# Performance work log

Hardware: AMD Instinct MI355X
Metric: run time of the kernel (lower is better)

Reference implementation:

```python
import jax, jax.numpy as jnp
import numpy as np
import math

N = 256  # channels == model dim M
B, H, W = 8, 48, 48
EPS = 1e-5


def _kaiming(key, shape, a=math.sqrt(5)):
    # kaiming_normal_ with fan_in = shape[1] (2D weight), leaky_relu gain
    fan_in = shape[1]
    gain = math.sqrt(2.0 / (1.0 + a * a))
    std = gain / math.sqrt(fan_in)
    return std * jax.random.normal(key, shape, dtype=jnp.float32)


def setup_inputs() -> dict:
    key = jax.random.key(0)
    ks = jax.random.split(key, 6)
    x_l = jax.random.normal(ks[0], (B, N, H, W), dtype=jnp.float32)
    x_r = jax.random.normal(ks[1], (B, N, H, W), dtype=jnp.float32)
    Wq = _kaiming(ks[2], (N, N))
    Wk = _kaiming(ks[3], (N, N))
    Wv = _kaiming(ks[4], (N, N))
    Wo = _kaiming(ks[5], (N, N))
    g1 = jnp.ones((N,), jnp.float32); b1 = jnp.zeros((N,), jnp.float32)
    g2 = jnp.ones((N,), jnp.float32); b2 = jnp.zeros((N,), jnp.float32)
    return {"x_l": x_l, "x_r": x_r, "Wq": Wq, "Wk": Wk, "Wv": Wv, "Wo": Wo,
            "g1": g1, "b1": b1, "g2": g2, "b2": b2}


def _layernorm(x, g, b):
    mu = jnp.mean(x, axis=-1, keepdims=True)
    var = jnp.mean(jnp.square(x - mu), axis=-1, keepdims=True)
    return (x - mu) * jax.lax.rsqrt(var + EPS) * g + b


def reference(x_l, x_r, Wq, Wk, Wv, Wo, g1, b1, g2, b2):
    Bsz, C, Hh, Ww = x_l.shape
    S = Hh * Ww
    # [B, C, H, W] -> [B, S, C]
    xl = x_l.reshape(Bsz, C, S).transpose(0, 2, 1)
    xr = x_r.reshape(Bsz, C, S).transpose(0, 2, 1)
    xln_l = _layernorm(xl, g1, b1)
    xln_r = _layernorm(xr, g2, b2)
    Ql = xln_l @ Wq; Qr = xln_r @ Wq
    Kl = xln_l @ Wk; Kr = xln_r @ Wk
    Vl = xln_l @ Wv; Vr = xln_r @ Wv
    scale = 1.0 / math.sqrt(C)
    Al = jnp.einsum('bsc,btc->bst', Ql, Kr) * scale  # [B,S,S]
    Ar = jnp.einsum('bsc,btc->bst', Qr, Kl) * scale
    # NOTE: original uses nn.Softmax() with dim=None; for a 3-D tensor torch's
    # legacy _get_softmax_dim resolves to dim=0 (over batch). Faithfully replicated.
    Pl = jax.nn.softmax(Al, axis=0)
    Pr = jax.nn.softmax(Ar, axis=0)
    out_l = xl + (Pl @ Vl) @ Wo
    out_r = xr + (Pr @ Vr) @ Wo
    out_l = out_l.transpose(0, 2, 1).reshape(Bsz, C, Hh, Ww)
    out_r = out_r.transpose(0, 2, 1).reshape(Bsz, C, Hh, Ww)
    return out_l, out_r
```

## Files before the change

kernel.cpp:

```cpp
#include <hip/hip_runtime.h>
#include <stdint.h>

#define SDIM 2304
#define CDIM 256
#define NB   8
#define MTOT (NB * SDIM)

typedef __attribute__((ext_vector_type(8))) short short8;
typedef __attribute__((ext_vector_type(4))) float f32x4;

__device__ __forceinline__ float b2f(unsigned short h) {
  union { unsigned int u; float f; } v; v.u = ((unsigned int)h) << 16; return v.f;
}
__device__ __forceinline__ unsigned short f2b(float f) {
  union { unsigned int u; float f; } v; v.f = f;
  unsigned int u = v.u;
  u += 0x7fffu + ((u >> 16) & 1u);
  return (unsigned short)(u >> 16);
}
static inline unsigned short f2b_host(float f) {
  union { unsigned int u; float f; } v; v.f = f;
  unsigned int u = v.u;
  u += 0x7fffu + ((u >> 16) & 1u);
  return (unsigned short)(u >> 16);
}

__device__ __forceinline__ void gload_lds16(const unsigned short* g, unsigned short* l) {
  __builtin_amdgcn_global_load_lds(
      (const __attribute__((address_space(1))) unsigned int*)g,
      (__attribute__((address_space(3))) unsigned int*)l,
      16, 0, 0);
}

__global__ __launch_bounds__(64)
void detect_dtype(const unsigned short* __restrict__ x, int* __restrict__ flag)
{
  int lane = threadIdx.x;
  int bad = 0;
  for (int i = lane; i < 1024; i += 64) {
    float v = b2f(x[i]);
    if (!(fabsf(v) < 1e20f)) bad = 1;
  }
  unsigned long long m = __ballot(bad);
  if (lane == 0) flag[0] = (m != 0ULL) ? 1 : 0;
}

constexpr int EP_PLAIN = 0, EP_QKV = 1, EP_OUT = 2, EP_ACC = 3;

template <int EP, int SW>
__global__ __launch_bounds__(256, 2)
void gemm_nt(const unsigned short* __restrict__ pA, int lda, long sAz,
             const unsigned short* __restrict__ pB, int ldb, long sBz, int zx,
             unsigned short* __restrict__ pC, int ldc, long sCz,
             unsigned short* __restrict__ pQ, unsigned short* __restrict__ pK,
             unsigned short* __restrict__ pV,
             const unsigned short* __restrict__ pX0, const unsigned short* __restrict__ pX1,
             float* __restrict__ pFacc, unsigned short* __restrict__ pBf, int accmode,
             const int* __restrict__ dflag, int Kdim)
{
  __shared__ __align__(16) unsigned short As[3][128 * 32];
  __shared__ __align__(16) unsigned short Bs[3][128 * 32];

  const int tid = threadIdx.x;
  int bx, by, bz;
  if constexpr (SW == 1) {
    const int h = blockIdx.x;
    const int q = h >> 4, r = h & 15;
    const int p = q * 8 + (r & 7);
    by = r >> 3;
    bx = p % 18;
    bz = p / 18;
  } else {
    bx = blockIdx.x; by = blockIdx.y; bz = blockIdx.z;
  }
  const int z = bz;
  const long m0 = (long)bx * 128;
  const long n0 = (long)by * 128;
  const unsigned short* A  = pA + (long)z * sAz;
  const unsigned short* Bm = pB + (long)(z ^ zx) * sBz;

  const int lane = tid & 63;
  const int wave = tid >> 6;
  const int wm = (wave & 1) << 6;
  const int wn = (wave >> 1) << 6;
  const int lr = lane & 15;
  const int quad = lane >> 4;

  f32x4 acc[4][4];
#pragma unroll
  for (int i = 0; i < 4; ++i)
#pragma unroll
    for (int j = 0; j < 4; ++j) acc[i][j] = (f32x4)0.0f;

  const int e0 = tid, e1 = tid + 256;
  const int r0 = e0 >> 2, c0 = (e0 & 3) << 3;
  const int r1 = e1 >> 2, c1 = (e1 & 3) << 3;
  const unsigned short* pa0 = A  + (m0 + r0) * lda + c0;
  const unsigned short* pa1 = A  + (m0 + r1) * lda + c1;
  const unsigned short* pb0 = Bm + (n0 + r0) * ldb + c0;
  const unsigned short* pb1 = Bm + (n0 + r1) * ldb + c1;

  const int nt = Kdim >> 5;

  gload_lds16(pa0,      &As[0][e0 * 8]);
  gload_lds16(pa1,      &As[0][e1 * 8]);
  gload_lds16(pb0,      &Bs[0][e0 * 8]);
  gload_lds16(pb1,      &Bs[0][e1 * 8]);
  gload_lds16(pa0 + 32, &As[1][e0 * 8]);
  gload_lds16(pa1 + 32, &As[1][e1 * 8]);
  gload_lds16(pb0 + 32, &Bs[1][e0 * 8]);
  gload_lds16(pb1 + 32, &Bs[1][e1 * 8]);

  int bc = 0;
  for (int t = 0; t < nt; ++t) {
    if (t < nt - 1) asm volatile("s_waitcnt vmcnt(4)" ::: "memory");
    else            asm volatile("s_waitcnt vmcnt(0)" ::: "memory");
    __builtin_amdgcn_s_barrier();
    asm volatile("" ::: "memory");

    if (t + 2 < nt) {
      const int k2 = (t + 2) << 5;
      const int b2 = bc ? bc - 1 : 2;
      gload_lds16(pa0 + k2, &As[b2][e0 * 8]);
      gload_lds16(pa1 + k2, &As[b2][e1 * 8]);
      gload_lds16(pb0 + k2, &Bs[b2][e0 * 8]);
      gload_lds16(pb1 + k2, &Bs[b2][e1 * 8]);
    }

    short8 af[4], bfr[4];
#pragma unroll
    for (int i = 0; i < 4; ++i) {
      af[i]  = *(const short8*)&As[bc][(wm + i * 16 + lr) * 32 + quad * 8];
      bfr[i] = *(const short8*)&Bs[bc][(wn + i * 16 + lr) * 32 + quad * 8];
    }
#pragma unroll
    for (int i = 0; i < 4; ++i)
#pragma unroll
      for (int j = 0; j < 4; ++j)
        acc[i][j] = __builtin_amdgcn_mfma_f32_16x16x32_bf16(af[i], bfr[j], acc[i][j], 0, 0, 0);

    bc = (bc == 2) ? 0 : bc + 1;
  }

  if constexpr (EP == EP_PLAIN) {
    unsigned short* Cp = pC + (long)z * sCz;
#pragma unroll
    for (int i = 0; i < 4; ++i) {
      const long mb = m0 + wm + i * 16 + quad * 4;
#pragma unroll
      for (int j = 0; j < 4; ++j) {
        const long n = n0 + wn + j * 16 + lr;
#pragma unroll
        for (int r = 0; r < 4; ++r)
          Cp[(mb + r) * ldc + n] = f2b(acc[i][j][r]);
      }
    }
  } else if constexpr (EP == EP_QKV) {
    const int g  = (int)(n0 >> 8);
    const int nb = (int)(n0 & 255);
    if (g < 2) {
      unsigned short* Cp = (g == 0 ? pQ : pK) + (long)z * sCz;
#pragma unroll
      for (int i = 0; i < 4; ++i) {
        const long mb = m0 + wm + i * 16 + quad * 4;
#pragma unroll
        for (int j = 0; j < 4; ++j) {
          const int n = nb + wn + j * 16 + lr;
#pragma unroll
          for (int r = 0; r < 4; ++r)
            Cp[(mb + r) * CDIM + n] = f2b(acc[i][j][r]);
        }
      }
    } else {
      const int b = (int)(m0 / SDIM);
      const int sblk = (int)(m0 % SDIM);
      unsigned short* Vz = pV + ((long)z * NB + b) * (long)CDIM * SDIM;
#pragma unroll
      for (int i = 0; i < 4; ++i) {
        const int s = sblk + wm + i * 16 + quad * 4;
#pragma unroll
        for (int j = 0; j < 4; ++j) {
          const int c = nb + wn + j * 16 + lr;
          ushort4 pk;
          pk.x = f2b(acc[i][j][0]); pk.y = f2b(acc[i][j][1]);
          pk.z = f2b(acc[i][j][2]); pk.w = f2b(acc[i][j][3]);
          *(ushort4*)&Vz[(long)c * SDIM + s] = pk;
        }
      }
    }
  } else if constexpr (EP == EP_ACC) {
    float* Fz = pFacc + (long)z * SDIM * CDIM;
    unsigned short* Bz = pBf + (long)z * SDIM * CDIM;
#pragma unroll
    for (int i = 0; i < 4; ++i) {
      const long mb = m0 + wm + i * 16 + quad * 4;
#pragma unroll
      for (int j = 0; j < 4; ++j) {
        const long n = n0 + wn + j * 16 + lr;
#pragma unroll
        for (int r = 0; r < 4; ++r) {
          const long idx = (mb + r) * CDIM + n;
          float v = acc[i][j][r];
          if (accmode != 0) v += Fz[idx];
          if (accmode == 2) Bz[idx] = f2b(v);
          else              Fz[idx] = v;
        }
      }
    }
  } else {
    const int io32 = dflag[0];
    const int b = (int)(m0 / SDIM);
    const int sblk = (int)(m0 % SDIM);
    const unsigned short* Xraw = (z == 0 ? pX0 : pX1);
    if (io32) {
      const float* Xf = (const float*)Xraw + (long)b * CDIM * SDIM;
      float* Of = (float*)pC + (long)z * sCz + (long)b * CDIM * SDIM;
#pragma unroll
      for (int i = 0; i < 4; ++i) {
        const int s = sblk + wm + i * 16 + quad * 4;
#pragma unroll
        for (int j = 0; j < 4; ++j) {
          const int c = (int)n0 + wn + j * 16 + lr;
          const long off = (long)c * SDIM + s;
          float4 rx = *(const float4*)&Xf[off];
          float4 pk;
          pk.x = acc[i][j][0] + rx.x;
          pk.y = acc[i][j][1] + rx.y;
          pk.z = acc[i][j][2] + rx.z;
          pk.w = acc[i][j][3] + rx.w;
          *(float4*)&Of[off] = pk;
        }
      }
    } else {
      const unsigned short* X = Xraw + (long)b * CDIM * SDIM;
      unsigned short* O = pC + (long)z * sCz + (long)b * CDIM * SDIM;
#pragma unroll
      for (int i = 0; i < 4; ++i) {
        const int s = sblk + wm + i * 16 + quad * 4;
#pragma unroll
        for (int j = 0; j < 4; ++j) {
          const int c = (int)n0 + wn + j * 16 + lr;
          const long off = (long)c * SDIM + s;
          ushort4 rx = *(const ushort4*)&X[off];
          ushort4 pk;
          pk.x = f2b(acc[i][j][0] + b2f(rx.x));
          pk.y = f2b(acc[i][j][1] + b2f(rx.y));
          pk.z = f2b(acc[i][j][2] + b2f(rx.z));
          pk.w = f2b(acc[i][j][3] + b2f(rx.w));
          *(ushort4*)&O[off] = pk;
        }
      }
    }
  }
}

__global__ __launch_bounds__(256)
void wtrans(const unsigned short* __restrict__ Wq, const unsigned short* __restrict__ Wk,
            const unsigned short* __restrict__ Wv, const unsigned short* __restrict__ Wo,
            unsigned short* __restrict__ WT, const int* __restrict__ dflag)
{
  const int io32 = dflag[0];
  int idx = blockIdx.x * 256 + threadIdx.x;
  int w = idx >> 16, r = idx & 65535, n = r >> 8, k = r & 255;
  const unsigned short* W = (w == 0) ? Wq : (w == 1) ? Wk : (w == 2) ? Wv : Wo;
  float v = io32 ? ((const float*)W)[k * 256 + n] : b2f(W[k * 256 + n]);
  if (w == 0) v *= 0.0625f;
  WT[w * 65536 + n * 256 + k] = f2b(v);
}

__global__ __launch_bounds__(256)
void ln_kernel(const unsigned short* __restrict__ xl, const unsigned short* __restrict__ xr,
               const unsigned short* __restrict__ g1, const unsigned short* __restrict__ b1,
               const unsigned short* __restrict__ g2, const unsigned short* __restrict__ b2,
               unsigned short* __restrict__ XLN, const int* __restrict__ dflag)
{
  const int io32 = dflag[0];
  const int strm = blockIdx.z;
  const int b = blockIdx.y;
  const int s0 = blockIdx.x * 64;
  const unsigned short* xraw = (strm ? xr : xl);
  const float*          xf = (const float*)xraw + (long)b * CDIM * SDIM;
  const unsigned short* xh = xraw + (long)b * CDIM * SDIM;
  const unsigned short* gg = strm ? g2 : g1;
  const unsigned short* bb = strm ? b2 : b1;
  const int tid = threadIdx.x;
  const int sl = tid & 63;
  const int team = tid >> 6;

  __shared__ float red[2][4][64];
  __shared__ float muS[64], rsS[64];
  __shared__ __align__(16) unsigned short tile[64 * 258];

  float sum = 0.f, sq = 0.f;
  for (int c = team * 64; c < team * 64 + 64; ++c) {
    const long off = (long)c * SDIM + s0 + sl;
    float v = io32 ? xf[off] : b2f(xh[off]);
    sum += v; sq += v * v;
  }
  red[0][team][sl] = sum; red[1][team][sl] = sq;
  __syncthreads();
  if (tid < 64) {
    float s_ = red[0][0][tid] + red[0][1][tid] + red[0][2][tid] + red[0][3][tid];
    float q_ = red[1][0][tid] + red[1][1][tid] + red[1][2][tid] + red[1][3][tid];
    float mu = s_ * (1.0f / CDIM);
    float var = q_ * (1.0f / CDIM) - mu * mu;
    muS[tid] = mu;
    rsS[tid] = rsqrtf(var + 1e-5f);
  }
  __syncthreads();
  const float mu = muS[sl], rs = rsS[sl];
  for (int c = team * 64; c < team * 64 + 64; ++c) {
    const long off = (long)c * SDIM + s0 + sl;
    float v = io32 ? xf[off] : b2f(xh[off]);
    float gv = io32 ? ((const float*)gg)[c] : b2f(gg[c]);
    float bv = io32 ? ((const float*)bb)[c] : b2f(bb[c]);
    tile[sl * 258 + c] = f2b((v - mu) * rs * gv + bv);
  }
  __syncthreads();
  unsigned short* outp = XLN + ((long)strm * MTOT + (long)b * SDIM + s0) * CDIM;
  const ushort2* t2 = (const ushort2*)tile;
  ushort2* o2 = (ushort2*)outp;
#pragma unroll
  for (int i = 0; i < 32; ++i) {
    int idx = i * 256 + tid;
    int r = idx >> 7, c2 = idx & 127;
    o2[idx] = t2[r * 129 + c2];
  }
}

__global__ __launch_bounds__(256)
void softmax_bdim(unsigned short* __restrict__ Ab, long total)
{
  const int strm = blockIdx.y;
  const long i8 = (((long)blockIdx.x << 8) + threadIdx.x) << 3;
  unsigned short* base = Ab + (long)strm * NB * total + i8;
  float v[NB][8];
#pragma unroll
  for (int b = 0; b < NB; ++b) {
    const ushort4* p = (const ushort4*)(base + (long)b * total);
    ushort4 a0 = p[0], a1 = p[1];
    v[b][0] = b2f(a0.x); v[b][1] = b2f(a0.y); v[b][2] = b2f(a0.z); v[b][3] = b2f(a0.w);
    v[b][4] = b2f(a1.x); v[b][5] = b2f(a1.y); v[b][6] = b2f(a1.z); v[b][7] = b2f(a1.w);
  }
#pragma unroll
  for (int j = 0; j < 8; ++j) {
    float mx = v[0][j];
#pragma unroll
    for (int b = 1; b < NB; ++b) mx = fmaxf(mx, v[b][j]);
    float s = 0.f;
#pragma unroll
    for (int b = 0; b < NB; ++b) { float e = __expf(v[b][j] - mx); v[b][j] = e; s += e; }
    float inv = 1.0f / s;
#pragma unroll
    for (int b = 0; b < NB; ++b) v[b][j] *= inv;
  }
#pragma unroll
  for (int b = 0; b < NB; ++b) {
    ushort4 a0, a1;
    a0.x = f2b(v[b][0]); a0.y = f2b(v[b][1]); a0.z = f2b(v[b][2]); a0.w = f2b(v[b][3]);
    a1.x = f2b(v[b][4]); a1.y = f2b(v[b][5]); a1.z = f2b(v[b][6]); a1.w = f2b(v[b][7]);
    ushort4* p = (ushort4*)(base + (long)b * total);
    p[0] = a0; p[1] = a1;
  }
}

__global__ __launch_bounds__(256)
void fill_val(unsigned short* __restrict__ out, unsigned short v, int n)
{
  int i = blockIdx.x * 256 + threadIdx.x;
  if (i < n) out[i] = v;
}

extern "C" void kernel_launch(void* const* d_in, const int* in_sizes, int n_in,
                              void* d_out, int out_size, void* d_ws, size_t ws_size,
                              hipStream_t stream)
{
  const unsigned short* xl = (const unsigned short*)d_in[0];
  const unsigned short* xr = (const unsigned short*)d_in[1];
  const unsigned short* Wq = (const unsigned short*)d_in[2];
  const unsigned short* Wk = (const unsigned short*)d_in[3];
  const unsigned short* Wv = (const unsigned short*)d_in[4];
  const unsigned short* Wo = (const unsigned short*)d_in[5];
  const unsigned short* g1 = (const unsigned short*)d_in[6];
  const unsigned short* b1 = (const unsigned short*)d_in[7];
  const unsigned short* g2 = (const unsigned short*)d_in[8];
  const unsigned short* b2 = (const unsigned short*)d_in[9];
  unsigned short* out = (unsigned short*)d_out;

  const size_t need_chunk = 113770496UL + 64;
  const size_t need_full  = 227016704UL + 64;
  if (ws_size < need_chunk) {
    float wsmb = (float)(ws_size >> 20);
    unsigned short v = f2b_host(wsmb * 100.0f);
    fill_val<<<dim3((out_size + 255) / 256), 256, 0, stream>>>(out, v, out_size);
    return;
  }

  int* dFlag = (int*)((char*)d_ws + ((ws_size - 16) & ~15UL));
  detect_dtype<<<dim3(1), 64, 0, stream>>>(xl, dFlag);

  if (ws_size >= need_full) {
    unsigned short* WT  = (unsigned short*)d_ws;
    unsigned short* Qb  = WT + 262144L;
    unsigned short* Kb  = Qb + 9437184L;
    unsigned short* Vt  = Kb + 9437184L;
    unsigned short* Ab  = Vt + 9437184L;
    unsigned short* XLN = Ab;
    unsigned short* PVbf = Qb;

    wtrans<<<dim3(1024), 256, 0, stream>>>(Wq, Wk, Wv, Wo, WT, dFlag);
    ln_kernel<<<dim3(36, 8, 2), 256, 0, stream>>>(xl, xr, g1, b1, g2, b2, XLN, dFlag);

    gemm_nt<EP_QKV, 0><<<dim3(144, 6, 2), 256, 0, stream>>>(
        XLN, CDIM, (long)MTOT * CDIM,
        WT, CDIM, 0L, 0,
        nullptr, 0, (long)MTOT * CDIM,
        Qb, Kb, Vt, nullptr, nullptr,
        nullptr, nullptr, 0, dFlag, CDIM);

    gemm_nt<EP_PLAIN, 0><<<dim3(18, 18, 16), 256, 0, stream>>>(
        Qb, CDIM, (long)SDIM * CDIM,
        Kb, CDIM, (long)SDIM * CDIM, 8,
        Ab, SDIM, (long)SDIM * SDIM,
        nullptr, nullptr, nullptr, nullptr, nullptr,
        nullptr, nullptr, 0, dFlag, CDIM);

    softmax_bdim<<<dim3(2592, 2), 256, 0, stream>>>(Ab, (long)SDIM * SDIM);

    gemm_nt<EP_PLAIN, 1><<<dim3(576), 256, 0, stream>>>(
        Ab, SDIM, (long)SDIM * SDIM,
        Vt, SDIM, (long)CDIM * SDIM, 0,
        PVbf, CDIM, (long)SDIM * CDIM,
        nullptr, nullptr, nullptr, nullptr, nullptr,
        nullptr, nullptr, 0, dFlag, SDIM);

    gemm_nt<EP_OUT, 0><<<dim3(144, 2, 2), 256, 0, stream>>>(
        PVbf, CDIM, (long)MTOT * CDIM,
        WT + 768L * 256, CDIM, 0L, 0,
        out, 0, (long)NB * CDIM * SDIM,
        nullptr, nullptr, nullptr, xl, xr,
        nullptr, nullptr, 0, dFlag, CDIM);
    return;
  }

  unsigned short* WT  = (unsigned short*)d_ws;
  unsigned short* XLN = WT  + 1024L * 256;
  unsigned short* Abc = XLN;
  unsigned short* Qb  = XLN + 9437184L;
  unsigned short* Kb  = Qb  + 9437184L;
  unsigned short* Vt  = Kb  + 9437184L;
  float*          PVacc = (float*)(Vt + 9437184L);
  unsigned short* PVbf  = Qb;

  wtrans<<<dim3(1024), 256, 0, stream>>>(Wq, Wk, Wv, Wo, WT, dFlag);
  ln_kernel<<<dim3(36, 8, 2), 256, 0, stream>>>(xl, xr, g1, b1, g2, b2, XLN, dFlag);

  gemm_nt<EP_QKV, 0><<<dim3(144, 6, 2), 256, 0, stream>>>(
      XLN, CDIM, (long)MTOT * CDIM,
      WT, CDIM, 0L, 0,
      nullptr, 0, (long)MTOT * CDIM,
      Qb, Kb, Vt, nullptr, nullptr,
      nullptr, nullptr, 0, dFlag, CDIM);

  for (int tc = 0; tc < 9; ++tc) {
    gemm_nt<EP_PLAIN, 0><<<dim3(18, 2, 16), 256, 0, stream>>>(
        Qb, CDIM, (long)SDIM * CDIM,
        Kb + (long)tc * 256 * CDIM, CDIM, (long)SDIM * CDIM, 8,
        Abc, 256, (long)SDIM * 256,
        nullptr, nullptr, nullptr, nullptr, nullptr,
        nullptr, nullptr, 0, dFlag, CDIM);

    softmax_bdim<<<dim3(288, 2), 256, 0, stream>>>(Abc, (long)SDIM * 256);

    const int mode = (tc == 0) ? 0 : (tc == 8) ? 2 : 1;
    gemm_nt<EP_ACC, 0><<<dim3(18, 2, 16), 256, 0, stream>>>(
        Abc, 256, (long)SDIM * 256,
        Vt + (long)tc * 256, SDIM, (long)CDIM * SDIM, 0,
        nullptr, 0, 0L,
        nullptr, nullptr, nullptr, nullptr, nullptr,
        PVacc, PVbf, mode, dFlag, 256);
  }

  gemm_nt<EP_OUT, 0><<<dim3(144, 2, 2), 256, 0, stream>>>(
      PVbf, CDIM, (long)MTOT * CDIM,
      WT + 768L * 256, CDIM, 0L, 0,
      out, 0, (long)NB * CDIM * SDIM,
      nullptr, nullptr, nullptr, xl, xr,
      nullptr, nullptr, 0, dFlag, CDIM);
}
```

Measured before the change: 388.7 us.

## Fuse QK^T GEMM with batch-dim softmax into a single kernel

Replaces the separate QK^T GEMM and batch-axis softmax kernels with one kernel. Each block computes a 128x64 score tile for all 8 batches, keeps the bf16 results packed in registers, applies the softmax over the batch dimension in registers, and writes the probabilities once. This removes one full write-and-reread round trip of the large score tensor. In exchange it uses many registers (the packed score array across 8 batches), which may lower occupancy, and the final stores are scalar 2-byte writes rather than vectorized ones.

```diff
diff --git a/kernel.cpp b/kernel.cpp
--- a/kernel.cpp
+++ b/kernel.cpp
@@ -249,6 +249,134 @@
           pk.w = f2b(acc[i][j][3] + b2f(rx.w));
           *(ushort4*)&O[off] = pk;
         }
+      }
+    }
+  }
+}
+
+__global__ __launch_bounds__(256, 2)
+void qk_softmax(const unsigned short* __restrict__ pQ,
+                const unsigned short* __restrict__ pK,
+                unsigned short* __restrict__ pAb)
+{
+  __shared__ __align__(16) unsigned short As[3][128 * 32];
+  __shared__ __align__(16) unsigned short Bs[3][64 * 32];
+
+  const int tid = threadIdx.x;
+  const int strm = blockIdx.z;
+  const long m0 = (long)blockIdx.x * 128;
+  const long n0 = (long)blockIdx.y * 64;
+
+  const int lane = tid & 63;
+  const int wave = tid >> 6;
+  const int wm = (wave & 1) << 6;
+  const int wn = (wave >> 1) << 5;
+  const int lr = lane & 15;
+  const int quad = lane >> 4;
+
+  const long bstr = (long)SDIM * CDIM;
+  const unsigned short* Qs = pQ + (long)(strm * 8) * bstr;
+  const unsigned short* Ks = pK + (long)((strm ^ 1) * 8) * bstr;
+
+  const int e0 = tid, e1 = tid + 256;
+  const int ra0 = e0 >> 2, ca0 = (e0 & 3) << 3;
+  const int ra1 = e1 >> 2, ca1 = (e1 & 3) << 3;
+  const unsigned short* pa0 = Qs + (m0 + ra0) * CDIM + ca0;
+  const unsigned short* pa1 = Qs + (m0 + ra1) * CDIM + ca1;
+  const unsigned short* pb0 = Ks + (n0 + ra0) * CDIM + ca0;
+
+  auto stage = [&](int u) {
+    const long off = (long)(u >> 3) * bstr + (long)((u & 7) << 5);
+    const int sl = u % 3;
+    gload_lds16(pa0 + off, &As[sl][e0 * 8]);
+    gload_lds16(pa1 + off, &As[sl][e1 * 8]);
+    gload_lds16(pb0 + off, &Bs[sl][tid * 8]);
+  };
+
+  stage(0); stage(1);
+
+  unsigned int ps[8][16];
+  f32x4 acc[4][2];
+#pragma unroll
+  for (int i = 0; i < 4; ++i)
+#pragma unroll
+    for (int j = 0; j < 2; ++j) acc[i][j] = (f32x4)0.0f;
+
+#pragma unroll
+  for (int b = 0; b < 8; ++b) {
+#pragma unroll
+    for (int t = 0; t < 8; ++t) {
+      const int u = b * 8 + t;
+      if (u < 63) asm volatile("s_waitcnt vmcnt(3)" ::: "memory");
+      else        asm volatile("s_waitcnt vmcnt(0)" ::: "memory");
+      __builtin_amdgcn_s_barrier();
+      asm volatile("" ::: "memory");
+
+      if (u + 2 < 64) stage(u + 2);
+
+      const int sl = u % 3;
+      short8 af[4], bfr[2];
+#pragma unroll
+      for (int i = 0; i < 4; ++i)
+        af[i] = *(const short8*)&As[sl][(wm + i * 16 + lr) * 32 + quad * 8];
+#pragma unroll
+      for (int j = 0; j < 2; ++j)
+        bfr[j] = *(const short8*)&Bs[sl][(wn + j * 16 + lr) * 32 + quad * 8];
+#pragma unroll
+      for (int i = 0; i < 4; ++i)
+#pragma unroll
+        for (int j = 0; j < 2; ++j)
+          acc[i][j] = __builtin_amdgcn_mfma_f32_16x16x32_bf16(af[i], bfr[j], acc[i][j], 0, 0, 0);
+    }
+#pragma unroll
+    for (int i = 0; i < 4; ++i)
+#pragma unroll
+      for (int j = 0; j < 2; ++j) {
+        ps[b][(i * 2 + j) * 2]     = (unsigned)f2b(acc[i][j][0]) | ((unsigned)f2b(acc[i][j][1]) << 16);
+        ps[b][(i * 2 + j) * 2 + 1] = (unsigned)f2b(acc[i][j][2]) | ((unsigned)f2b(acc[i][j][3]) << 16);
+        acc[i][j] = (f32x4)0.0f;
+      }
+  }
+
+#pragma unroll
+  for (int s = 0; s < 16; ++s) {
+    float lo[8], hi[8];
+#pragma unroll
+    for (int b = 0; b < 8; ++b) {
+      lo[b] = b2f((unsigned short)(ps[b][s] & 0xffffu));
+      hi[b] = b2f((unsigned short)(ps[b][s] >> 16));
+    }
+    float mlo = lo[0], mhi = hi[0];
+#pragma unroll
+    for (int b = 1; b < 8; ++b) { mlo = fmaxf(mlo, lo[b]); mhi = fmaxf(mhi, hi[b]); }
+    float slo = 0.f, shi = 0.f;
+#pragma unroll
+    for (int b = 0; b < 8; ++b) {
+      lo[b] = __expf(lo[b] - mlo); slo += lo[b];
+      hi[b] = __expf(hi[b] - mhi); shi += hi[b];
+    }
+    const float ilo = 1.0f / slo, ihi = 1.0f / shi;
+#pragma unroll
+    for (int b = 0; b < 8; ++b)
+      ps[b][s] = (unsigned)f2b(lo[b] * ilo) | ((unsigned)f2b(hi[b] * ihi) << 16);
+  }
+
+  unsigned short* Ab0 = pAb + (long)(strm * 8) * ((long)SDIM * SDIM);
+#pragma unroll
+  for (int b = 0; b < 8; ++b) {
+    unsigned short* Az = Ab0 + (long)b * SDIM * SDIM;
+#pragma unroll
+    for (int i = 0; i < 4; ++i) {
+      const long mb = m0 + wm + i * 16 + quad * 4;
+#pragma unroll
+      for (int j = 0; j < 2; ++j) {
+        const long n = n0 + wn + j * 16 + lr;
+        const int si = (i * 2 + j) * 2;
+        const unsigned p0 = ps[b][si], p1 = ps[b][si + 1];
+        Az[(mb + 0) * SDIM + n] = (unsigned short)(p0 & 0xffffu);
+        Az[(mb + 1) * SDIM + n] = (unsigned short)(p0 >> 16);
+        Az[(mb + 2) * SDIM + n] = (unsigned short)(p1 & 0xffffu);
+        Az[(mb + 3) * SDIM + n] = (unsigned short)(p1 >> 16);
       }
     }
   }
@@ -418,14 +546,7 @@
         Qb, Kb, Vt, nullptr, nullptr,
         nullptr, nullptr, 0, dFlag, CDIM);
 
-    gemm_nt<EP_PLAIN, 0><<<dim3(18, 18, 16), 256, 0, stream>>>(
-        Qb, CDIM, (long)SDIM * CDIM,
-        Kb, CDIM, (long)SDIM * CDIM, 8,
-        Ab, SDIM, (long)SDIM * SDIM,
-        nullptr, nullptr, nullptr, nullptr, nullptr,
-        nullptr, nullptr, 0, dFlag, CDIM);
-
-    softmax_bdim<<<dim3(2592, 2), 256, 0, stream>>>(Ab, (long)SDIM * SDIM);
+    qk_softmax<<<dim3(18, 36, 2), 256, 0, stream>>>(Qb, Kb, Ab);
 
     gemm_nt<EP_PLAIN, 1><<<dim3(576), 256, 0, stream>>>(
         Ab, SDIM, (long)SDIM * SDIM,
```

Result: slower. 472.0 us (+21.4%).

## Deepen GEMM LDS pipeline to four stages, swizzle LDS, remap QK grid

Applied to the files above, without the earlier changes.

The shared GEMM kernel moves from a 3-stage to a 4-stage cp.async-style LDS ring with three tiles in flight and adjusted vmcnt waits. It also XOR-swizzles the 16-byte chunk placement in LDS to cut bank conflicts on the fragment reads, and raises wave priority around the MFMA block. The QK^T GEMM gets a 1-D grid with a remapping that spreads consecutive blocks across XCDs. LDS use grows to 64KB per block, which still allows two blocks per CU but leaves less headroom.

```diff
diff --git a/kernel.cpp b/kernel.cpp
--- a/kernel.cpp
+++ b/kernel.cpp
@@ -58,8 +58,8 @@
              float* __restrict__ pFacc, unsigned short* __restrict__ pBf, int accmode,
              const int* __restrict__ dflag, int Kdim)
 {
-  __shared__ __align__(16) unsigned short As[3][128 * 32];
-  __shared__ __align__(16) unsigned short Bs[3][128 * 32];
+  __shared__ __align__(16) unsigned short As[4][128 * 32];
+  __shared__ __align__(16) unsigned short Bs[4][128 * 32];
 
   const int tid = threadIdx.x;
   int bx, by, bz;
@@ -70,6 +70,10 @@
     by = r >> 3;
     bx = p % 18;
     bz = p / 18;
+  } else if constexpr (SW == 2) {
+    const int b = blockIdx.x;
+    const int n = (b & 7) * 648 + (b >> 3);
+    bz = n / 324; const int r = n % 324; by = r / 18; bx = r % 18;
   } else {
     bx = blockIdx.x; by = blockIdx.y; bz = blockIdx.z;
   }
@@ -93,53 +97,57 @@
     for (int j = 0; j < 4; ++j) acc[i][j] = (f32x4)0.0f;
 
   const int e0 = tid, e1 = tid + 256;
-  const int r0 = e0 >> 2, c0 = (e0 & 3) << 3;
-  const int r1 = e1 >> 2, c1 = (e1 & 3) << 3;
+  const int r0 = e0 >> 2, c0 = (((e0 & 3) ^ ((r0 >> 1) & 3)) << 3);
+  const int r1 = e1 >> 2, c1 = (((e1 & 3) ^ ((r1 >> 1) & 3)) << 3);
   const unsigned short* pa0 = A  + (m0 + r0) * lda + c0;
   const unsigned short* pa1 = A  + (m0 + r1) * lda + c1;
   const unsigned short* pb0 = Bm + (n0 + r0) * ldb + c0;
   const unsigned short* pb1 = Bm + (n0 + r1) * ldb + c1;
 
+  const int chunk = quad ^ ((lr >> 1) & 3);
+  int aoff[4], boff[4];
+#pragma unroll
+  for (int i = 0; i < 4; ++i) {
+    aoff[i] = (wm + i * 16 + lr) * 32 + chunk * 8;
+    boff[i] = (wn + i * 16 + lr) * 32 + chunk * 8;
+  }
+
   const int nt = Kdim >> 5;
 
-  gload_lds16(pa0,      &As[0][e0 * 8]);
-  gload_lds16(pa1,      &As[0][e1 * 8]);
-  gload_lds16(pb0,      &Bs[0][e0 * 8]);
-  gload_lds16(pb1,      &Bs[0][e1 * 8]);
-  gload_lds16(pa0 + 32, &As[1][e0 * 8]);
-  gload_lds16(pa1 + 32, &As[1][e1 * 8]);
-  gload_lds16(pb0 + 32, &Bs[1][e0 * 8]);
-  gload_lds16(pb1 + 32, &Bs[1][e1 * 8]);
-
-  int bc = 0;
+  auto stage = [&](int kt) {
+    const int sl = kt & 3;
+    const int k = kt << 5;
+    gload_lds16(pa0 + k, &As[sl][e0 * 8]);
+    gload_lds16(pa1 + k, &As[sl][e1 * 8]);
+    gload_lds16(pb0 + k, &Bs[sl][e0 * 8]);
+    gload_lds16(pb1 + k, &Bs[sl][e1 * 8]);
+  };
+
+  stage(0); stage(1); stage(2);
+
   for (int t = 0; t < nt; ++t) {
-    if (t < nt - 1) asm volatile("s_waitcnt vmcnt(4)" ::: "memory");
-    else            asm volatile("s_waitcnt vmcnt(0)" ::: "memory");
+    if (t < nt - 2)       asm volatile("s_waitcnt vmcnt(8)" ::: "memory");
+    else if (t == nt - 2) asm volatile("s_waitcnt vmcnt(4)" ::: "memory");
+    else                  asm volatile("s_waitcnt vmcnt(0)" ::: "memory");
     __builtin_amdgcn_s_barrier();
     asm volatile("" ::: "memory");
 
-    if (t + 2 < nt) {
-      const int k2 = (t + 2) << 5;
-      const int b2 = bc ? bc - 1 : 2;
-      gload_lds16(pa0 + k2, &As[b2][e0 * 8]);
-      gload_lds16(pa1 + k2, &As[b2][e1 * 8]);
-      gload_lds16(pb0 + k2, &Bs[b2][e0 * 8]);
-      gload_lds16(pb1 + k2, &Bs[b2][e1 * 8]);
+    if (t + 3 < nt) stage(t + 3);
+
+    const int sl = t & 3;
+    short8 af[4], bfr[4];
+#pragma unroll
+    for (int i = 0; i < 4; ++i) {
+      af[i]  = *(const short8*)&As[sl][aoff[i]];
+      bfr[i] = *(const short8*)&Bs[sl][boff[i]];
     }
-
-    short8 af[4], bfr[4];
-#pragma unroll
-    for (int i = 0; i < 4; ++i) {
-      af[i]  = *(const short8*)&As[bc][(wm + i * 16 + lr) * 32 + quad * 8];
-      bfr[i] = *(const short8*)&Bs[bc][(wn + i * 16 + lr) * 32 + quad * 8];
-    }
+    __builtin_amdgcn_s_setprio(1);
 #pragma unroll
     for (int i = 0; i < 4; ++i)
 #pragma unroll
       for (int j = 0; j < 4; ++j)
         acc[i][j] = __builtin_amdgcn_mfma_f32_16x16x32_bf16(af[i], bfr[j], acc[i][j], 0, 0, 0);
-
-    bc = (bc == 2) ? 0 : bc + 1;
+    __builtin_amdgcn_s_setprio(0);
   }
 
   if constexpr (EP == EP_PLAIN) {
@@ -418,7 +426,7 @@
         Qb, Kb, Vt, nullptr, nullptr,
         nullptr, nullptr, 0, dFlag, CDIM);
 
-    gemm_nt<EP_PLAIN, 0><<<dim3(18, 18, 16), 256, 0, stream>>>(
+    gemm_nt<EP_PLAIN, 2><<<dim3(5184), 256, 0, stream>>>(
         Qb, CDIM, (long)SDIM * CDIM,
         Kb, CDIM, (long)SDIM * CDIM, 8,
         Ab, SDIM, (long)SDIM * SDIM,
```

After: 427.9 us. 10.1% more time.
